# Optimization experiments

Hardware: AMD Instinct MI355X
Metric: run time of the kernel (lower is better)

Reference implementation:

```python
import jax, jax.numpy as jnp
import numpy as np


def setup_inputs() -> dict:
    key = jax.random.key(0)
    k1, k2, k3, k4 = jax.random.split(key, 4)
    B, T, N, D = 16, 4, 1601, 1280  # batch, max_num_tiles, tokens/tile, embed_dim
    x = jax.random.normal(k1, (B, T, N, D), dtype=jnp.float32)
    # (h_tiles, w_tiles) per sample, each in [1, 2] so h*w <= max_num_tiles=4
    aspect_ratio = jax.random.randint(k2, (B, 2), 1, 3, dtype=jnp.int64)
    embedding = jax.random.normal(k3, (T, T, 1, D), dtype=jnp.float32) / np.sqrt(D)
    gate = jnp.zeros((1,), dtype=jnp.float32) + 0.1  # nonzero so output depends on embedding
    return {"x": x, "aspect_ratio": aspect_ratio, "embedding": embedding, "gate": gate}


def reference(x, aspect_ratio, embedding, gate):
    # x: (B, T, N, D); embedding: (T, T, 1, D); aspect_ratio: (B, 2) ints
    B, T, N, D = x.shape
    t = jnp.arange(T)[None, :]                    # (1, T) flattened tile index
    h = aspect_ratio[:, 0:1]                      # (B, 1)
    w = aspect_ratio[:, 1:2]                      # (B, 1)
    valid = t < h * w                             # (B, T) tile is non-padded
    row = jnp.where(valid, t // w, 0)             # (B, T)
    col = jnp.where(valid, t % w, 0)              # (B, T)
    pe = embedding[row, col]                      # (B, T, 1, D) gathered pos embeds
    pe = jnp.where(valid[:, :, None, None], pe, jnp.zeros((), x.dtype))
    return x + pe * jnp.tanh(gate)                # broadcast over N tokens
```

## Files before the change

### kernel.cpp

```cpp
#include <hip/hip_runtime.h>
#include <math.h>

#define Bsz 16
#define Tsz 4
#define Nsz 1601
#define Dsz 1280
#define D4  (Dsz / 4)
#define GRIDX 24

typedef float f32x4 __attribute__((ext_vector_type(4)));

__device__ __forceinline__ void load_hw(const int* __restrict__ ar, int b, int& h, int& w) {
    int v0 = ar[2 * b];
    int v1 = ar[2 * b + 1];
    if (v1 != 0) {
        h = v0; w = v1;
    } else {
        h = ar[4 * b];
        w = ar[4 * b + 2];
    }
}

__global__ void add_pe_kernel(const f32x4* __restrict__ x,
                              const f32x4* __restrict__ emb,
                              const int* __restrict__ ar,
                              const float* __restrict__ gate,
                              f32x4* __restrict__ out) {
    int bt = blockIdx.y;
    int b = bt >> 2;
    int t = bt & 3;
    int h, w;
    load_hw(ar, b, h, w);
    float tg = tanhf(gate[0]);
    f32x4 pv = (f32x4)(0.f);
    if (t < h * w) {
        int row = t / w;
        int col = t % w;
        pv = emb[(row * Tsz + col) * D4 + threadIdx.x] * tg;
    }

    const long stride = (long)GRIDX * D4;
    long off = (long)bt * Nsz * D4 + (long)blockIdx.x * D4 + threadIdx.x;
    const long end = ((long)bt + 1) * Nsz * D4;

    for (; off + stride < end; off += 2 * stride) {
        f32x4 a = x[off];
        f32x4 c = x[off + stride];
        a += pv;
        c += pv;
        out[off] = a;
        out[off + stride] = c;
    }
    if (off < end) {
        f32x4 a = x[off];
        a += pv;
        out[off] = a;
    }
}

extern "C" void kernel_launch(void* const* d_in, const int* in_sizes, int n_in,
                              void* d_out, int out_size, void* d_ws, size_t ws_size,
                              hipStream_t stream) {
    const f32x4* x    = (const f32x4*)d_in[0];
    const int*   ar   = (const int*)d_in[1];
    const f32x4* emb  = (const f32x4*)d_in[2];
    const float* gate = (const float*)d_in[3];
    f32x4* out = (f32x4*)d_out;

    add_pe_kernel<<<dim3(GRIDX, Bsz * Tsz), D4, 0, stream>>>(x, emb, ar, gate, out);
}
```

Before: 220.6 us.

## Precompute gated PE table and use flat grid for broadcast add

Result: faster. 181.1 us, median of 2 (-17.9%).

```diff
diff --git a/kernel.cpp b/kernel.cpp
--- a/kernel.cpp
+++ b/kernel.cpp
@@ -6,7 +6,10 @@
 #define Nsz 1601
 #define Dsz 1280
 #define D4  (Dsz / 4)
-#define GRIDX 24
+#define SLAB (Nsz * D4)
+#define TOTAL4 (Bsz * Tsz * SLAB)
+#define EPT 2
+#define BLK 256
 
 typedef float f32x4 __attribute__((ext_vector_type(4)));
 
@@ -21,41 +24,38 @@
     }
 }
 
-__global__ void add_pe_kernel(const f32x4* __restrict__ x,
-                              const f32x4* __restrict__ emb,
-                              const int* __restrict__ ar,
-                              const float* __restrict__ gate,
-                              f32x4* __restrict__ out) {
-    int bt = blockIdx.y;
+__global__ void build_pe_kernel(const f32x4* __restrict__ emb,
+                                const int* __restrict__ ar,
+                                const float* __restrict__ gate,
+                                f32x4* __restrict__ pe) {
+    int bt = blockIdx.x;
     int b = bt >> 2;
     int t = bt & 3;
     int h, w;
     load_hw(ar, b, h, w);
     float tg = tanhf(gate[0]);
-    f32x4 pv = (f32x4)(0.f);
+    f32x4 v = (f32x4)(0.f);
     if (t < h * w) {
         int row = t / w;
         int col = t % w;
-        pv = emb[(row * Tsz + col) * D4 + threadIdx.x] * tg;
+        v = emb[(row * Tsz + col) * D4 + threadIdx.x] * tg;
     }
+    pe[bt * D4 + threadIdx.x] = v;
+}
 
-    const long stride = (long)GRIDX * D4;
-    long off = (long)bt * Nsz * D4 + (long)blockIdx.x * D4 + threadIdx.x;
-    const long end = ((long)bt + 1) * Nsz * D4;
-
-    for (; off + stride < end; off += 2 * stride) {
-        f32x4 a = x[off];
-        f32x4 c = x[off + stride];
-        a += pv;
-        c += pv;
-        out[off] = a;
-        out[off + stride] = c;
-    }
-    if (off < end) {
-        f32x4 a = x[off];
-        a += pv;
-        out[off] = a;
-    }
+__global__ void add_pe_flat_kernel(const f32x4* __restrict__ x,
+                                   const f32x4* __restrict__ pe,
+                                   f32x4* __restrict__ out) {
+    unsigned i0 = blockIdx.x * (BLK * EPT) + threadIdx.x;
+    unsigned i1 = i0 + BLK;
+    f32x4 a0 = x[i0];
+    f32x4 a1 = x[i1];
+    unsigned p0i = (i0 / (unsigned)SLAB) * (unsigned)D4 + i0 % (unsigned)D4;
+    unsigned p1i = (i1 / (unsigned)SLAB) * (unsigned)D4 + i1 % (unsigned)D4;
+    f32x4 p0 = pe[p0i];
+    f32x4 p1 = pe[p1i];
+    out[i0] = a0 + p0;
+    out[i1] = a1 + p1;
 }
 
 extern "C" void kernel_launch(void* const* d_in, const int* in_sizes, int n_in,
@@ -67,5 +67,7 @@
     const float* gate = (const float*)d_in[3];
     f32x4* out = (f32x4*)d_out;
 
-    add_pe_kernel<<<dim3(GRIDX, Bsz * Tsz), D4, 0, stream>>>(x, emb, ar, gate, out);
+    f32x4* pe = (f32x4*)d_ws;
+    build_pe_kernel<<<dim3(Bsz * Tsz), D4, 0, stream>>>(emb, ar, gate, pe);
+    add_pe_flat_kernel<<<dim3(TOTAL4 / (BLK * EPT)), BLK, 0, stream>>>(x, pe, out);
 }
```
